# Kernel optimization log

Measured on AMD Instinct MI355X. Metric: run time of the kernel, lower is better.

Reference implementation:

```python
import jax, jax.numpy as jnp
import numpy as np

B, T, D, H, L = 4, 512, 768, 12, 12
HD = D // H
DFF = int(D * 4 * 2 / 3)  # 2048, SwiGLU hidden per source
VOCAB = 50257
NMEM, TOPK, NLAT = 1024, 8, 4
CAP = max(1, int(T * 0.125))  # MoD capacity = 64
MOD = [i % 2 == 1 for i in range(L)]  # get_mod_layers()


def setup_inputs():
    key = jax.random.key(0)
    ks = iter(jax.random.split(key, 40))
    def w(shape, s=0.02):
        return jax.random.normal(next(ks), shape, jnp.float32) * s
    return {
        'input_ids': jax.random.randint(next(ks), (B, T), 0, VOCAB),
        'embed_w': w((VOCAB, D)),
        'pos_w': w((T, D)),
        'qkv_w': w((L, 3 * D, D)),
        'out_w': w((L, D, D)),
        'norm1_w': jnp.ones((L, D), jnp.float32),
        'norm2_w': jnp.ones((L, D), jnp.float32),
        'ff_w1': w((L, DFF, D)),
        'ff_w2': w((L, DFF, D)),
        'ff_w3': w((L, D, DFF)),
        'router_w': w((L, D)),
        'lat_qkv_w': w((3 * D, D)),
        'lat_out_w': w((D, D)),
        'lat_norm1_w': jnp.ones((D,), jnp.float32),
        'lat_norm2_w': jnp.ones((D,), jnp.float32),
        'lat_ff_w1': w((DFF, D)),
        'lat_ff_w2': w((DFF, D)),
        'lat_ff_w3': w((D, DFF)),
        'mem_keys': w((NMEM, D)),
        'mem_values': w((NMEM, D)),
        'mem_qp': w((D, D)),
        'mem_op': w((D, D)),
        'gate_w1': w((D // 2, 2 * D)),
        'gate_b1': jnp.zeros((D // 2,), jnp.float32),
        'gate_w2': w((1, D // 2)),
        'gate_b2': jnp.zeros((1,), jnp.float32),
        'final_norm_w': jnp.ones((D,), jnp.float32),
    }


def rmsnorm(x, w):
    return x * jax.lax.rsqrt(jnp.mean(x * x, -1, keepdims=True) + 1e-6) * w


def attention(x, qkv_w, out_w):
    b, t, _ = x.shape
    qkv = (x @ qkv_w.T).reshape(b, t, 3, H, HD)
    q, k, v = jnp.moveaxis(qkv, 2, 0)  # each [b, t, H, HD]
    scores = jnp.einsum('bqhd,bkhd->bhqk', q, k) / np.float32(np.sqrt(HD))
    causal = jnp.triu(jnp.ones((t, t), bool), 1)
    scores = jnp.where(causal, -jnp.inf, scores)
    a = jax.nn.softmax(scores, axis=-1)
    o = jnp.einsum('bhqk,bkhd->bqhd', a, v).reshape(b, t, D)
    return o @ out_w.T


def tblock(x, qkv_w, out_w, n1, n2, w1, w2, w3):
    x = x + attention(rmsnorm(x, n1), qkv_w, out_w)
    h = rmsnorm(x, n2)
    return x + (jax.nn.silu(h @ w1.T) * (h @ w2.T)) @ w3.T


def _forward(input_ids, embed_w, pos_w, qkv_w, out_w, norm1_w, norm2_w, ff_w1, ff_w2,
             ff_w3, router_w, lat_qkv_w, lat_out_w, lat_norm1_w, lat_norm2_w,
             lat_ff_w1, lat_ff_w2, lat_ff_w3, mem_keys, mem_values, mem_qp, mem_op,
             gate_w1, gate_b1, gate_w2, gate_b2, final_norm_w):
    x = embed_w[input_ids] + pos_w[None, :T]  # [B, T, D]
    for i in range(L):
        p = (qkv_w[i], out_w[i], norm1_w[i], norm2_w[i], ff_w1[i], ff_w2[i], ff_w3[i])
        if MOD[i]:
            # MoD: top-k router selection; the source computes the full block
            # and keeps the processed value only at selected token positions.
            scores = x @ router_w[i]  # [B, T]
            _, idx = jax.lax.top_k(scores, CAP)
            sel = jnp.zeros((x.shape[0], T), bool).at[jnp.arange(x.shape[0])[:, None], idx].set(True)
            x = jnp.where(sel[..., None], tblock(x, *p), x)
        else:
            x = tblock(x, *p)
    # COCONUT-style latent reasoning: NLAT passes through a shared block
    for _ in range(NLAT):
        x = tblock(x, lat_qkv_w, lat_out_w, lat_norm1_w, lat_norm2_w,
                   lat_ff_w1, lat_ff_w2, lat_ff_w3)
    # kNN memory retrieval
    q = x @ mem_qp.T
    sim = jnp.einsum('btd,md->btm', q, mem_keys) / np.float32(np.sqrt(D))
    tk_sim, tk_idx = jax.lax.top_k(sim, TOPK)
    wts = jax.nn.softmax(tk_sim, axis=-1)
    vals = mem_values[tk_idx]  # [B, T, K, D] irregular gather
    retrieved = jnp.einsum('btk,btkd->btd', wts, vals) @ mem_op.T
    gi = jnp.concatenate([x, retrieved], axis=-1)
    gate = jax.nn.sigmoid(
        jax.nn.gelu(gi @ gate_w1.T + gate_b1, approximate=False) @ gate_w2.T + gate_b2)
    x = x + gate * retrieved
    return rmsnorm(x, final_norm_w) @ embed_w.T  # tied lm_head -> [B, T, VOCAB]


def reference(input_ids, embed_w, pos_w, qkv_w, out_w, norm1_w, norm2_w, ff_w1, ff_w2,
              ff_w3, router_w, lat_qkv_w, lat_out_w, lat_norm1_w, lat_norm2_w,
              lat_ff_w1, lat_ff_w2, lat_ff_w3, mem_keys, mem_values, mem_qp, mem_op,
              gate_w1, gate_b1, gate_w2, gate_b2, final_norm_w):
    return _forward(input_ids, embed_w, pos_w, qkv_w, out_w, norm1_w, norm2_w, ff_w1,
                    ff_w2, ff_w3, router_w, lat_qkv_w, lat_out_w, lat_norm1_w,
                    lat_norm2_w, lat_ff_w1, lat_ff_w2, lat_ff_w3, mem_keys,
                    mem_values, mem_qp, mem_op, gate_w1, gate_b1, gate_w2, gate_b2,
                    final_norm_w)
```

## Files before the change

### kernel.cpp

```cpp
#include <hip/hip_runtime.h>
#include <math.h>

#define BB 4
#define TT 512
#define DD 768
#define NH 12
#define HDIM 64
#define NL 12
#define DFF 2048
#define NVOCAB 50257
#define NMEM 1024
#define KTOP 8
#define NLAT 4
#define CAPK 64
#define NTOK (BB*TT)
#define NTOKD ((long)NTOK*DD)

typedef __attribute__((ext_vector_type(8))) short bf16x8;
typedef __attribute__((ext_vector_type(4))) float f32x4;


__device__ __forceinline__ unsigned bf16rne(float v) {
    unsigned u = __builtin_bit_cast(unsigned, v);
    return u + 0x7fffu + ((u >> 16) & 1u);
}

__device__ __forceinline__ void split4(const float4 v, uint2& hi, uint2& lo) {
    unsigned rx = bf16rne(v.x), ry = bf16rne(v.y);
    unsigned rz = bf16rne(v.z), rw_ = bf16rne(v.w);
    hi.x = (rx >> 16) | (ry & 0xffff0000u);
    hi.y = (rz >> 16) | (rw_ & 0xffff0000u);
    float dx = v.x - __builtin_bit_cast(float, rx & 0xffff0000u);
    float dy = v.y - __builtin_bit_cast(float, ry & 0xffff0000u);
    float dz = v.z - __builtin_bit_cast(float, rz & 0xffff0000u);
    float dw = v.w - __builtin_bit_cast(float, rw_ & 0xffff0000u);
    unsigned lx = bf16rne(dx), ly = bf16rne(dy);
    unsigned lz = bf16rne(dz), lw = bf16rne(dw);
    lo.x = (lx >> 16) | (ly & 0xffff0000u);
    lo.y = (lz >> 16) | (lw & 0xffff0000u);
}

template<int EPI>
__global__ __launch_bounds__(256, 2)
void gemm_nt(const float* __restrict__ A, const float* __restrict__ W,
             float* __restrict__ C, const float* __restrict__ aux,
             int M, int N, int K, int lda, int ldb, int ldc, float scale,
             int zdiv, long sAb, long sAh, long sBb, long sBh, long sCb, long sCh)
{
    __shared__ unsigned short As_hi[128][40];
    __shared__ unsigned short As_lo[128][40];
    __shared__ unsigned short Ws_hi[128][40];
    __shared__ unsigned short Ws_lo[128][40];

    const int z  = blockIdx.z;
    const int bz = z / zdiv, hz = z % zdiv;
    A += (long)bz*sAb + (long)hz*sAh;
    W += (long)bz*sBb + (long)hz*sBh;
    C += (long)bz*sCb + (long)hz*sCh;

    const int row0 = blockIdx.y * 128, col0 = blockIdx.x * 128;
    const int tid  = threadIdx.x;
    const int srow = tid >> 3;
    const int sc4  = (tid & 7) << 2;
    const int wid = tid >> 6, lane = tid & 63;
    const int wm = (wid >> 1) << 6, wn = (wid & 1) << 6;
    const int lr = lane & 15, lg = lane >> 4;

    f32x4 acc[4][4] = {};

    const float* Abase = A + (long)row0 * lda + sc4;
    const float* Wbase = W + (long)col0 * ldb + sc4;

    float4 ra[4], rw[4];
    auto loadk = [&](int kk) {
        #pragma unroll
        for (int j = 0; j < 4; ++j) {
            const int r = srow + (j << 5);
            ra[j] = *(const float4*)(Abase + (long)r * lda + kk);
            const int wr = col0 + r;
            if (wr < N) rw[j] = *(const float4*)(Wbase + (long)r * ldb + kk);
            else        rw[j] = make_float4(0.f, 0.f, 0.f, 0.f);
        }
    };
    loadk(0);

    for (int kk = 0; kk < K; kk += 32) {
        #pragma unroll
        for (int j = 0; j < 4; ++j) {
            const int r = srow + (j << 5);
            uint2 h, l;
            split4(ra[j], h, l);
            *(uint2*)&As_hi[r][sc4] = h;
            *(uint2*)&As_lo[r][sc4] = l;
            split4(rw[j], h, l);
            *(uint2*)&Ws_hi[r][sc4] = h;
            *(uint2*)&Ws_lo[r][sc4] = l;
        }
        __syncthreads();
        if (kk + 32 < K) loadk(kk + 32);

        bf16x8 ah[4], al[4], bh[4], bl[4];
        #pragma unroll
        for (int i = 0; i < 4; ++i) {
            ah[i] = *(const bf16x8*)&As_hi[wm + (i << 4) + lr][lg << 3];
            al[i] = *(const bf16x8*)&As_lo[wm + (i << 4) + lr][lg << 3];
            bh[i] = *(const bf16x8*)&Ws_hi[wn + (i << 4) + lr][lg << 3];
            bl[i] = *(const bf16x8*)&Ws_lo[wn + (i << 4) + lr][lg << 3];
        }
        #pragma unroll
        for (int i = 0; i < 4; ++i)
            #pragma unroll
            for (int j = 0; j < 4; ++j) {
                acc[i][j] = __builtin_amdgcn_mfma_f32_16x16x32_bf16(ah[i], bh[j], acc[i][j], 0, 0, 0);
                acc[i][j] = __builtin_amdgcn_mfma_f32_16x16x32_bf16(ah[i], bl[j], acc[i][j], 0, 0, 0);
                acc[i][j] = __builtin_amdgcn_mfma_f32_16x16x32_bf16(al[i], bh[j], acc[i][j], 0, 0, 0);
            }
        __syncthreads();
    }

    #pragma unroll
    for (int i = 0; i < 4; ++i) {
        #pragma unroll
        for (int j = 0; j < 4; ++j) {
            #pragma unroll
            for (int r = 0; r < 4; ++r) {
                const int m = row0 + wm + (i << 4) + (lg << 2) + r;
                const int n = col0 + wn + (j << 4) + lr;
                if (n >= N) continue;
                float v = acc[i][j][r];
                long idx = (long)m * ldc + n;
                if (EPI == 0)      C[idx] = v * scale;
                else if (EPI == 1) C[idx] = aux[idx] + v;
                else if (EPI == 2) { float u = v + aux[n];
                                     C[idx] = 0.5f*u*(1.f + erff(u*0.70710678118654752f)); }
                else               C[idx] = (n > m) ? -INFINITY : v * scale;
            }
        }
    }
}

__global__ __launch_bounds__(64)
void softmax_av_k(const float* __restrict__ scores, const float* __restrict__ qkv,
                  float* __restrict__ attno)
{
    const int q = blockIdx.x, h = blockIdx.y, b = blockIdx.z;
    const int lane = threadIdx.x;
    const float* srow = scores + ((long)(b*NH + h)*TT + q)*TT;
    __shared__ float p[TT];
    float loc[TT/64];
    float mx = -INFINITY;
    #pragma unroll
    for (int i=0;i<TT/64;i++){ loc[i] = srow[lane + (i<<6)]; mx = fmaxf(mx, loc[i]); }
    #pragma unroll
    for (int o=32;o;o>>=1) mx = fmaxf(mx, __shfl_xor(mx, o));
    float sum = 0.f;
    #pragma unroll
    for (int i=0;i<TT/64;i++){ loc[i] = expf(loc[i]-mx); sum += loc[i]; }
    #pragma unroll
    for (int o=32;o;o>>=1) sum += __shfl_xor(sum, o);
    const float inv = 1.f/sum;
    #pragma unroll
    for (int i=0;i<TT/64;i++) p[lane + (i<<6)] = loc[i]*inv;
    __syncthreads();
    const float* vbase = qkv + (long)b*TT*3*DD + 2*DD + h*HDIM + lane;
    float acc = 0.f;
    #pragma unroll 4
    for (int k=0;k<=q;k++) acc = fmaf(p[k], vbase[(long)k*3*DD], acc);
    attno[((long)b*TT + q)*DD + h*HDIM + lane] = acc;
}

__global__ __launch_bounds__(256)
void rmsnorm_k(const float* __restrict__ x, const float* __restrict__ w,
               float* __restrict__ y)
{
    const int row = blockIdx.x, tid = threadIdx.x;
    const float* xr = x + (long)row*DD;
    float s = 0.f;
    for (int j=tid;j<DD;j+=256){ float v = xr[j]; s = fmaf(v,v,s); }
    __shared__ float red[256];
    red[tid] = s; __syncthreads();
    for (int o=128;o;o>>=1){ if (tid<o) red[tid]+=red[tid+o]; __syncthreads(); }
    const float inv = rsqrtf(red[0]*(1.f/DD) + 1e-6f);
    for (int j=tid;j<DD;j+=256) y[(long)row*DD + j] = xr[j]*inv*w[j];
}

__global__ __launch_bounds__(256)
void router_k(const float* __restrict__ x, const float* __restrict__ rw,
              float* __restrict__ sc)
{
    const int row = blockIdx.x, tid = threadIdx.x;
    const float* xr = x + (long)row*DD;
    float s = 0.f;
    for (int j=tid;j<DD;j+=256) s = fmaf(xr[j], rw[j], s);
    __shared__ float red[256];
    red[tid] = s; __syncthreads();
    for (int o=128;o;o>>=1){ if (tid<o) red[tid]+=red[tid+o]; __syncthreads(); }
    if (tid==0) sc[row] = red[0];
}

__global__ __launch_bounds__(512)
void topk_mask_k(const float* __restrict__ sc, int* __restrict__ sel)
{
    const int b = blockIdx.x, t = threadIdx.x;
    __shared__ float v[TT]; __shared__ float rv[TT]; __shared__ int ri[TT];
    v[t] = sc[b*TT + t];
    sel[b*TT + t] = 0;
    __syncthreads();
    for (int it=0; it<CAPK; ++it){
        rv[t] = v[t]; ri[t] = t; __syncthreads();
        for (int o=256;o;o>>=1){
            if (t<o){
                if (rv[t+o] > rv[t] || (rv[t+o]==rv[t] && ri[t+o] < ri[t])){
                    rv[t]=rv[t+o]; ri[t]=ri[t+o];
                }
            }
            __syncthreads();
        }
        if (t==0){ sel[b*TT + ri[0]] = 1; v[ri[0]] = -INFINITY; }
        __syncthreads();
    }
}

__global__ void select_k(float* __restrict__ x, const float* __restrict__ xn,
                         const int* __restrict__ sel)
{
    const long i = (long)blockIdx.x*256 + threadIdx.x;
    if (sel[i/DD]) x[i] = xn[i];
}

__global__ void swiglu_k(float* __restrict__ h1, const float* __restrict__ h2)
{
    const long i = (long)blockIdx.x*256 + threadIdx.x;
    float a = h1[i];
    h1[i] = (a/(1.f+expf(-a))) * h2[i];
}

__global__ __launch_bounds__(64)
void knn_k(const float* __restrict__ sim, const float* __restrict__ mv,
           float* __restrict__ rpre)
{
    const int row = blockIdx.x, lane = threadIdx.x;
    __shared__ float sl[NMEM];
    for (int i=lane;i<NMEM;i+=64) sl[i] = sim[(long)row*NMEM + i];
    __syncthreads();
    float val8[KTOP]; int idx8[KTOP];
    for (int j=0;j<KTOP;j++){
        float bv = -INFINITY; int bi = NMEM;
        for (int i=lane;i<NMEM;i+=64){
            float vv = sl[i];
            if (vv > bv || (vv==bv && i < bi)){ bv=vv; bi=i; }
        }
        #pragma unroll
        for (int o=32;o;o>>=1){
            float ov = __shfl_xor(bv,o); int oi = __shfl_xor(bi,o);
            if (ov > bv || (ov==bv && oi < bi)){ bv=ov; bi=oi; }
        }
        val8[j]=bv; idx8[j]=bi;
        if (lane==0) sl[bi] = -INFINITY;
        __syncthreads();
    }
    const float mx = val8[0];
    float w8[KTOP]; float ssum = 0.f;
    #pragma unroll
    for (int j=0;j<KTOP;j++){ w8[j] = expf(val8[j]-mx); ssum += w8[j]; }
    const float inv = 1.f/ssum;
    for (int c=0;c<DD/64;c++){
        const int d = lane + (c<<6);
        float acc = 0.f;
        #pragma unroll
        for (int j=0;j<KTOP;j++) acc = fmaf(w8[j], mv[(long)idx8[j]*DD + d], acc);
        rpre[(long)row*DD + d] = acc*inv;
    }
}

__global__ void concat_k(const float* __restrict__ x, const float* __restrict__ r,
                         float* __restrict__ gi)
{
    const long i = (long)blockIdx.x*256 + threadIdx.x;
    const long row = i / (2*DD); const int c = (int)(i % (2*DD));
    gi[i] = (c < DD) ? x[row*DD + c] : r[row*DD + c - DD];
}

__global__ __launch_bounds__(256)
void gate2_k(const float* __restrict__ g1, const float* __restrict__ w2,
             const float* __restrict__ b2, float* __restrict__ gate)
{
    const int row  = blockIdx.x*4 + (threadIdx.x >> 6);
    const int lane = threadIdx.x & 63;
    const float* gr = g1 + (long)row*(DD/2);
    float s = 0.f;
    for (int j=lane;j<DD/2;j+=64) s = fmaf(gr[j], w2[j], s);
    #pragma unroll
    for (int o=32;o;o>>=1) s += __shfl_xor(s,o);
    if (lane==0) gate[row] = 1.f/(1.f+expf(-(s + b2[0])));
}

__global__ void gateadd_k(float* __restrict__ x, const float* __restrict__ r,
                          const float* __restrict__ gate)
{
    const long i = (long)blockIdx.x*256 + threadIdx.x;
    x[i] += gate[i/DD]*r[i];
}

__global__ void embed_k(const int* __restrict__ ids, const float* __restrict__ ew,
                        const float* __restrict__ pw, float* __restrict__ x)
{
    const long i = (long)blockIdx.x*256 + threadIdx.x;
    const long row = i / DD; const int d = (int)(i % DD); const int t = (int)(row % TT);
    x[i] = ew[(long)ids[row]*DD + d] + pw[(long)t*DD + d];
}

static void launch_gemm(hipStream_t s, int epi, const float* A, const float* W,
                        float* C, const float* aux, int M, int N, int K,
                        int lda, int ldb, int ldc, float scale,
                        int nz=1, int zdiv=1, long sAb=0, long sAh=0,
                        long sBb=0, long sBh=0, long sCb=0, long sCh=0)
{
    dim3 g((N+127)/128, M/128, nz), blk(256,1,1);
    switch (epi){
    case 0: gemm_nt<0><<<g,blk,0,s>>>(A,W,C,aux,M,N,K,lda,ldb,ldc,scale,zdiv,sAb,sAh,sBb,sBh,sCb,sCh); break;
    case 1: gemm_nt<1><<<g,blk,0,s>>>(A,W,C,aux,M,N,K,lda,ldb,ldc,scale,zdiv,sAb,sAh,sBb,sBh,sCb,sCh); break;
    case 2: gemm_nt<2><<<g,blk,0,s>>>(A,W,C,aux,M,N,K,lda,ldb,ldc,scale,zdiv,sAb,sAh,sBb,sBh,sCb,sCh); break;
    default:gemm_nt<3><<<g,blk,0,s>>>(A,W,C,aux,M,N,K,lda,ldb,ldc,scale,zdiv,sAb,sAh,sBb,sBh,sCb,sCh); break;
    }
}

struct Bufs { float *x2, *xnew, *hn, *attno, *qkv, *big; };

static void run_tblock(hipStream_t s, const float* qw, const float* ow,
                       const float* n1, const float* n2, const float* w1,
                       const float* w2, const float* w3,
                       const float* xin, float* xout, const Bufs& bf)
{
    rmsnorm_k<<<NTOK,256,0,s>>>(xin, n1, bf.hn);
    launch_gemm(s, 0, bf.hn, qw, bf.qkv, nullptr, NTOK, 3*DD, DD, DD, DD, 3*DD, 1.f);
    float* scores = bf.big;
    launch_gemm(s, 3, bf.qkv, bf.qkv + DD, scores, nullptr, TT, TT, HDIM,
                3*DD, 3*DD, TT, 0.125f,
                BB*NH, NH,
                (long)TT*3*DD, HDIM,
                (long)TT*3*DD, HDIM,
                (long)NH*TT*TT, (long)TT*TT);
    softmax_av_k<<<dim3(TT,NH,BB),64,0,s>>>(scores, bf.qkv, bf.attno);
    launch_gemm(s, 1, bf.attno, ow, bf.x2, xin, NTOK, DD, DD, DD, DD, DD, 1.f);
    rmsnorm_k<<<NTOK,256,0,s>>>(bf.x2, n2, bf.hn);
    float* h1 = bf.big; float* h2 = bf.big + (long)NTOK*DFF;
    launch_gemm(s, 0, bf.hn, w1, h1, nullptr, NTOK, DFF, DD, DD, DD, DFF, 1.f);
    launch_gemm(s, 0, bf.hn, w2, h2, nullptr, NTOK, DFF, DD, DD, DD, DFF, 1.f);
    swiglu_k<<<(NTOK*DFF)/256,256,0,s>>>(h1, h2);
    launch_gemm(s, 1, h1, w3, xout, bf.x2, NTOK, DD, DFF, DFF, DFF, DD, 1.f);
}

extern "C" void kernel_launch(void* const* d_in, const int* in_sizes, int n_in,
                              void* d_out, int out_size, void* d_ws, size_t ws_size,
                              hipStream_t stream)
{
    const int*   ids        = (const int*)  d_in[0];
    const float* embed_w    = (const float*)d_in[1];
    const float* pos_w      = (const float*)d_in[2];
    const float* qkv_w      = (const float*)d_in[3];
    const float* out_w      = (const float*)d_in[4];
    const float* norm1_w    = (const float*)d_in[5];
    const float* norm2_w    = (const float*)d_in[6];
    const float* ff_w1      = (const float*)d_in[7];
    const float* ff_w2      = (const float*)d_in[8];
    const float* ff_w3      = (const float*)d_in[9];
    const float* router_w   = (const float*)d_in[10];
    const float* lat_qkv_w  = (const float*)d_in[11];
    const float* lat_out_w  = (const float*)d_in[12];
    const float* lat_n1     = (const float*)d_in[13];
    const float* lat_n2     = (const float*)d_in[14];
    const float* lat_w1     = (const float*)d_in[15];
    const float* lat_w2     = (const float*)d_in[16];
    const float* lat_w3     = (const float*)d_in[17];
    const float* mem_keys   = (const float*)d_in[18];
    const float* mem_values = (const float*)d_in[19];
    const float* mem_qp     = (const float*)d_in[20];
    const float* mem_op     = (const float*)d_in[21];
    const float* gate_w1    = (const float*)d_in[22];
    const float* gate_b1    = (const float*)d_in[23];
    const float* gate_w2    = (const float*)d_in[24];
    const float* gate_b2    = (const float*)d_in[25];
    const float* fnorm_w    = (const float*)d_in[26];
    float* out = (float*)d_out;

    float* ws = (float*)d_ws;
    float* x     = ws;
    Bufs bf;
    bf.x2    = x        + NTOKD;
    bf.xnew  = bf.x2    + NTOKD;
    bf.hn    = bf.xnew  + NTOKD;
    bf.attno = bf.hn    + NTOKD;
    bf.qkv   = bf.attno + NTOKD;
    bf.big   = bf.qkv   + 3*NTOKD;
    float* rsc   = bf.big + (long)BB*NH*TT*TT;
    float* gateb = rsc + NTOK;
    int*   sel   = (int*)(gateb + NTOK);

    embed_k<<<(int)(NTOKD/256),256,0,stream>>>(ids, embed_w, pos_w, x);

    for (int i=0;i<NL;i++){
        const float* qw = qkv_w + (long)i*3*DD*DD;
        const float* ow = out_w + (long)i*DD*DD;
        const float* n1 = norm1_w + (long)i*DD;
        const float* n2 = norm2_w + (long)i*DD;
        const float* w1 = ff_w1 + (long)i*DFF*DD;
        const float* w2 = ff_w2 + (long)i*DFF*DD;
        const float* w3 = ff_w3 + (long)i*DD*DFF;
        if (i & 1){
            router_k<<<NTOK,256,0,stream>>>(x, router_w + (long)i*DD, rsc);
            topk_mask_k<<<BB,TT,0,stream>>>(rsc, sel);
            run_tblock(stream, qw,ow,n1,n2,w1,w2,w3, x, bf.xnew, bf);
            select_k<<<(int)(NTOKD/256),256,0,stream>>>(x, bf.xnew, sel);
        } else {
            run_tblock(stream, qw,ow,n1,n2,w1,w2,w3, x, x, bf);
        }
    }
    for (int r=0;r<NLAT;r++)
        run_tblock(stream, lat_qkv_w, lat_out_w, lat_n1, lat_n2,
                   lat_w1, lat_w2, lat_w3, x, x, bf);

    float* qmem = bf.qkv;
    float* rpre = bf.qkv + NTOKD;
    float* retr = bf.qkv + 2*NTOKD;
    launch_gemm(stream, 0, x, mem_qp, qmem, nullptr, NTOK, DD, DD, DD, DD, DD, 1.f);
    float* sim = bf.big;
    launch_gemm(stream, 0, qmem, mem_keys, sim, nullptr, NTOK, NMEM, DD, DD, DD, NMEM,
                0.036084391824351615f );
    knn_k<<<NTOK,64,0,stream>>>(sim, mem_values, rpre);
    launch_gemm(stream, 0, rpre, mem_op, retr, nullptr, NTOK, DD, DD, DD, DD, DD, 1.f);

    float* gi = bf.big + (long)NTOK*NMEM;
    concat_k<<<(int)((long)NTOK*2*DD/256),256,0,stream>>>(x, retr, gi);
    float* g1 = gi + (long)NTOK*2*DD;
    launch_gemm(stream, 2, gi, gate_w1, g1, gate_b1, NTOK, DD/2, 2*DD, 2*DD, 2*DD, DD/2, 1.f);
    gate2_k<<<NTOK/4,256,0,stream>>>(g1, gate_w2, gate_b2, gateb);
    gateadd_k<<<(int)(NTOKD/256),256,0,stream>>>(x, retr, gateb);

    rmsnorm_k<<<NTOK,256,0,stream>>>(x, fnorm_w, bf.hn);
    launch_gemm(stream, 0, bf.hn, embed_w, out, nullptr, NTOK, NVOCAB, DD, DD, DD, NVOCAB, 1.f);
}
```

Baseline: 8.302 ms.

## Restructure GEMM shared-memory staging, add 64-row tiles and streaming lm_head stores

The GEMM now stores tiles in shared memory in k-chunk-major order, so each thread writes a whole 16-byte vector. The hi/lo bf16 split uses a byte-permute truncation instead of round-to-nearest arithmetic, which cuts conversion ALU work. Very slightly less accurate splits are the trade-off. A 64-row tile variant is chosen automatically when the 128-tile grid would have fewer than 512 blocks, to improve occupancy on small GEMMs. The final vocab projection uses nontemporal stores so its large logits output does not pollute the cache.

New measurement: 8.325 ms. No clear change (+0.3%).

```diff
diff --git a/kernel.cpp b/kernel.cpp
--- a/kernel.cpp
+++ b/kernel.cpp
@@ -20,37 +20,47 @@
 typedef __attribute__((ext_vector_type(4))) float f32x4;
 
 
-__device__ __forceinline__ unsigned bf16rne(float v) {
-    unsigned u = __builtin_bit_cast(unsigned, v);
-    return u + 0x7fffu + ((u >> 16) & 1u);
-}
-
-__device__ __forceinline__ void split4(const float4 v, uint2& hi, uint2& lo) {
-    unsigned rx = bf16rne(v.x), ry = bf16rne(v.y);
-    unsigned rz = bf16rne(v.z), rw_ = bf16rne(v.w);
-    hi.x = (rx >> 16) | (ry & 0xffff0000u);
-    hi.y = (rz >> 16) | (rw_ & 0xffff0000u);
-    float dx = v.x - __builtin_bit_cast(float, rx & 0xffff0000u);
-    float dy = v.y - __builtin_bit_cast(float, ry & 0xffff0000u);
-    float dz = v.z - __builtin_bit_cast(float, rz & 0xffff0000u);
-    float dw = v.w - __builtin_bit_cast(float, rw_ & 0xffff0000u);
-    unsigned lx = bf16rne(dx), ly = bf16rne(dy);
-    unsigned lz = bf16rne(dz), lw = bf16rne(dw);
-    lo.x = (lx >> 16) | (ly & 0xffff0000u);
-    lo.y = (lz >> 16) | (lw & 0xffff0000u);
-}
-
-template<int EPI>
+__device__ __forceinline__ unsigned pack_hi2(float a, float b) {
+    return __builtin_amdgcn_perm(__builtin_bit_cast(unsigned, b),
+                                 __builtin_bit_cast(unsigned, a), 0x07060302u);
+}
+__device__ __forceinline__ float trunchi(float a) {
+    return __builtin_bit_cast(float, __builtin_bit_cast(unsigned, a) & 0xffff0000u);
+}
+
+__device__ __forceinline__ void cvt_store(unsigned short* hp, unsigned short* lp,
+                                          int str, int c, int r,
+                                          float4 e0, float4 e1)
+{
+    uint4 h, l;
+    h.x = pack_hi2(e0.x, e0.y);
+    h.y = pack_hi2(e0.z, e0.w);
+    h.z = pack_hi2(e1.x, e1.y);
+    h.w = pack_hi2(e1.z, e1.w);
+    float d0 = e0.x - trunchi(e0.x), d1 = e0.y - trunchi(e0.y);
+    float d2 = e0.z - trunchi(e0.z), d3 = e0.w - trunchi(e0.w);
+    float d4 = e1.x - trunchi(e1.x), d5 = e1.y - trunchi(e1.y);
+    float d6 = e1.z - trunchi(e1.z), d7 = e1.w - trunchi(e1.w);
+    l.x = pack_hi2(d0, d1); l.y = pack_hi2(d2, d3);
+    l.z = pack_hi2(d4, d5); l.w = pack_hi2(d6, d7);
+    *(uint4*)&hp[c*str + r*8] = h;
+    *(uint4*)&lp[c*str + r*8] = l;
+}
+
+template<int EPI, int TM>
 __global__ __launch_bounds__(256, 2)
 void gemm_nt(const float* __restrict__ A, const float* __restrict__ W,
              float* __restrict__ C, const float* __restrict__ aux,
              int M, int N, int K, int lda, int ldb, int ldc, float scale,
              int zdiv, long sAb, long sAh, long sBb, long sBh, long sCb, long sCh)
 {
-    __shared__ unsigned short As_hi[128][40];
-    __shared__ unsigned short As_lo[128][40];
-    __shared__ unsigned short Ws_hi[128][40];
-    __shared__ unsigned short Ws_lo[128][40];
+    constexpr int ASTR = TM*8 + 16;
+    constexpr int WSTR = 128*8 + 16;
+    constexpr int MI   = TM/32;
+    __shared__ __align__(16) unsigned short As_hi[4*ASTR];
+    __shared__ __align__(16) unsigned short As_lo[4*ASTR];
+    __shared__ __align__(16) unsigned short Ws_hi[4*WSTR];
+    __shared__ __align__(16) unsigned short Ws_lo[4*WSTR];
 
     const int z  = blockIdx.z;
     const int bz = z / zdiv, hz = z % zdiv;
@@ -58,57 +68,60 @@
     W += (long)bz*sBb + (long)hz*sBh;
     C += (long)bz*sCb + (long)hz*sCh;
 
-    const int row0 = blockIdx.y * 128, col0 = blockIdx.x * 128;
+    const int row0 = blockIdx.y * TM, col0 = blockIdx.x * 128;
     const int tid  = threadIdx.x;
-    const int srow = tid >> 3;
-    const int sc4  = (tid & 7) << 2;
     const int wid = tid >> 6, lane = tid & 63;
-    const int wm = (wid >> 1) << 6, wn = (wid & 1) << 6;
+    const int wm = (wid >> 1) * (TM/2), wn = (wid & 1) << 6;
     const int lr = lane & 15, lg = lane >> 4;
 
-    f32x4 acc[4][4] = {};
-
-    const float* Abase = A + (long)row0 * lda + sc4;
-    const float* Wbase = W + (long)col0 * ldb + sc4;
+    const int wr  = tid >> 1, wcb = (tid & 1) << 1;
+    const int ar  = (TM==128) ? (tid >> 1) : (tid >> 2);
+    const int acb = (TM==128) ? ((tid & 1) << 1) : (tid & 3);
+    constexpr int nAld = (TM==128) ? 4 : 2;
+
+    f32x4 acc[MI][4] = {};
+
+    const float* Abase = A + (long)(row0 + ar)*lda + acb*8;
+    const float* Wbase = W + (long)(col0 + wr)*ldb + wcb*8;
+    const bool wok = (col0 + wr) < N;
 
     float4 ra[4], rw[4];
     auto loadk = [&](int kk) {
         #pragma unroll
-        for (int j = 0; j < 4; ++j) {
-            const int r = srow + (j << 5);
-            ra[j] = *(const float4*)(Abase + (long)r * lda + kk);
-            const int wr = col0 + r;
-            if (wr < N) rw[j] = *(const float4*)(Wbase + (long)r * ldb + kk);
-            else        rw[j] = make_float4(0.f, 0.f, 0.f, 0.f);
-        }
+        for (int j = 0; j < nAld; ++j)
+            ra[j] = *(const float4*)(Abase + kk + 4*j);
+        #pragma unroll
+        for (int j = 0; j < 4; ++j)
+            rw[j] = wok ? *(const float4*)(Wbase + kk + 4*j)
+                        : make_float4(0.f, 0.f, 0.f, 0.f);
     };
     loadk(0);
 
     for (int kk = 0; kk < K; kk += 32) {
-        #pragma unroll
-        for (int j = 0; j < 4; ++j) {
-            const int r = srow + (j << 5);
-            uint2 h, l;
-            split4(ra[j], h, l);
-            *(uint2*)&As_hi[r][sc4] = h;
-            *(uint2*)&As_lo[r][sc4] = l;
-            split4(rw[j], h, l);
-            *(uint2*)&Ws_hi[r][sc4] = h;
-            *(uint2*)&Ws_lo[r][sc4] = l;
-        }
+        if (TM == 128) {
+            cvt_store(As_hi, As_lo, ASTR, acb,   ar, ra[0], ra[1]);
+            cvt_store(As_hi, As_lo, ASTR, acb+1, ar, ra[2], ra[3]);
+        } else {
+            cvt_store(As_hi, As_lo, ASTR, acb,   ar, ra[0], ra[1]);
+        }
+        cvt_store(Ws_hi, Ws_lo, WSTR, wcb,   wr, rw[0], rw[1]);
+        cvt_store(Ws_hi, Ws_lo, WSTR, wcb+1, wr, rw[2], rw[3]);
         __syncthreads();
         if (kk + 32 < K) loadk(kk + 32);
 
-        bf16x8 ah[4], al[4], bh[4], bl[4];
-        #pragma unroll
-        for (int i = 0; i < 4; ++i) {
-            ah[i] = *(const bf16x8*)&As_hi[wm + (i << 4) + lr][lg << 3];
-            al[i] = *(const bf16x8*)&As_lo[wm + (i << 4) + lr][lg << 3];
-            bh[i] = *(const bf16x8*)&Ws_hi[wn + (i << 4) + lr][lg << 3];
-            bl[i] = *(const bf16x8*)&Ws_lo[wn + (i << 4) + lr][lg << 3];
-        }
-        #pragma unroll
-        for (int i = 0; i < 4; ++i)
+        bf16x8 ah[MI], al[MI], bh[4], bl[4];
+        #pragma unroll
+        for (int i = 0; i < MI; ++i) {
+            ah[i] = *(const bf16x8*)&As_hi[lg*ASTR + (wm + (i<<4) + lr)*8];
+            al[i] = *(const bf16x8*)&As_lo[lg*ASTR + (wm + (i<<4) + lr)*8];
+        }
+        #pragma unroll
+        for (int j = 0; j < 4; ++j) {
+            bh[j] = *(const bf16x8*)&Ws_hi[lg*WSTR + (wn + (j<<4) + lr)*8];
+            bl[j] = *(const bf16x8*)&Ws_lo[lg*WSTR + (wn + (j<<4) + lr)*8];
+        }
+        #pragma unroll
+        for (int i = 0; i < MI; ++i)
             #pragma unroll
             for (int j = 0; j < 4; ++j) {
                 acc[i][j] = __builtin_amdgcn_mfma_f32_16x16x32_bf16(ah[i], bh[j], acc[i][j], 0, 0, 0);
@@ -119,7 +132,7 @@
     }
 
     #pragma unroll
-    for (int i = 0; i < 4; ++i) {
+    for (int i = 0; i < MI; ++i) {
         #pragma unroll
         for (int j = 0; j < 4; ++j) {
             #pragma unroll
@@ -133,7 +146,8 @@
                 else if (EPI == 1) C[idx] = aux[idx] + v;
                 else if (EPI == 2) { float u = v + aux[n];
                                      C[idx] = 0.5f*u*(1.f + erff(u*0.70710678118654752f)); }
-                else               C[idx] = (n > m) ? -INFINITY : v * scale;
+                else if (EPI == 3) C[idx] = (n > m) ? -INFINITY : v * scale;
+                else               __builtin_nontemporal_store(v * scale, &C[idx]);
             }
         }
     }
@@ -316,13 +330,28 @@
                         int nz=1, int zdiv=1, long sAb=0, long sAh=0,
                         long sBb=0, long sBh=0, long sCb=0, long sCh=0)
 {
-    dim3 g((N+127)/128, M/128, nz), blk(256,1,1);
-    switch (epi){
-    case 0: gemm_nt<0><<<g,blk,0,s>>>(A,W,C,aux,M,N,K,lda,ldb,ldc,scale,zdiv,sAb,sAh,sBb,sBh,sCb,sCh); break;
-    case 1: gemm_nt<1><<<g,blk,0,s>>>(A,W,C,aux,M,N,K,lda,ldb,ldc,scale,zdiv,sAb,sAh,sBb,sBh,sCb,sCh); break;
-    case 2: gemm_nt<2><<<g,blk,0,s>>>(A,W,C,aux,M,N,K,lda,ldb,ldc,scale,zdiv,sAb,sAh,sBb,sBh,sCb,sCh); break;
-    default:gemm_nt<3><<<g,blk,0,s>>>(A,W,C,aux,M,N,K,lda,ldb,ldc,scale,zdiv,sAb,sAh,sBb,sBh,sCb,sCh); break;
-    }
+    const long blocks128 = (long)((N+127)/128) * (M/128) * nz;
+    const int TM = (blocks128 < 512) ? 64 : 128;
+    dim3 g((N+127)/128, M/TM, nz), blk(256,1,1);
+#define GLAUNCH(E,T) gemm_nt<E,T><<<g,blk,0,s>>>(A,W,C,aux,M,N,K,lda,ldb,ldc,scale,zdiv,sAb,sAh,sBb,sBh,sCb,sCh)
+    if (TM == 128) {
+        switch (epi){
+        case 0: GLAUNCH(0,128); break;
+        case 1: GLAUNCH(1,128); break;
+        case 2: GLAUNCH(2,128); break;
+        case 3: GLAUNCH(3,128); break;
+        default:GLAUNCH(4,128); break;
+        }
+    } else {
+        switch (epi){
+        case 0: GLAUNCH(0,64); break;
+        case 1: GLAUNCH(1,64); break;
+        case 2: GLAUNCH(2,64); break;
+        case 3: GLAUNCH(3,64); break;
+        default:GLAUNCH(4,64); break;
+        }
+    }
+#undef GLAUNCH
 }
 
 struct Bufs { float *x2, *xnew, *hn, *attno, *qkv, *big; };
@@ -438,5 +467,5 @@
     gateadd_k<<<(int)(NTOKD/256),256,0,stream>>>(x, retr, gateb);
 
     rmsnorm_k<<<NTOK,256,0,stream>>>(x, fnorm_w, bf.hn);
-    launch_gemm(stream, 0, bf.hn, embed_w, out, nullptr, NTOK, NVOCAB, DD, DD, DD, NVOCAB, 1.f);
-}
+    launch_gemm(stream, 4, bf.hn, embed_w, out, nullptr, NTOK, NVOCAB, DD, DD, DD, NVOCAB, 1.f);
+}
```
